# Kernel tuning notes

Measured on AMD Instinct MI355X. Metric: run time of the kernel, lower is better.

## Reference

```python
import jax, jax.numpy as jnp
import numpy as np

D_MODEL = 256
NUM_UNIVERSES = 8
D_UNIVERSE = D_MODEL // NUM_UNIVERSES
B, S = 1, 1024
TEMP = 5.0
NEG = -1e9


def setup_inputs() -> dict:
    key = jax.random.key(0)
    ks = jax.random.split(key, 5)
    scale = 1.0 / np.sqrt(D_MODEL)
    return {
        "x": jax.random.normal(ks[0], (B, S, D_MODEL), dtype=jnp.float32),
        "Wq": jax.random.normal(ks[1], (D_MODEL, D_MODEL), dtype=jnp.float32) * scale,
        "bq": jnp.zeros((D_MODEL,), dtype=jnp.float32),
        "Wk": jax.random.normal(ks[2], (D_MODEL, D_MODEL), dtype=jnp.float32) * scale,
        "bk": jnp.zeros((D_MODEL,), dtype=jnp.float32),
        "Wv": jax.random.normal(ks[3], (D_MODEL, D_MODEL), dtype=jnp.float32) * scale,
        "bv": jnp.zeros((D_MODEL,), dtype=jnp.float32),
        "Wo": jax.random.normal(ks[4], (D_MODEL, D_MODEL), dtype=jnp.float32) * scale,
        "bo": jnp.zeros((D_MODEL,), dtype=jnp.float32),
    }


def reference(x, Wq, bq, Wk, bk, Wv, bv, Wo, bo):
    b, s, d = x.shape
    h, du = NUM_UNIVERSES, D_UNIVERSE
    # Projections; Q,K squashed to [0,1] fuzzy truth values
    Q = jax.nn.sigmoid(x @ Wq + bq)
    K = jax.nn.sigmoid(x @ Wk + bk)
    V = x @ Wv + bv
    # [B,S,D] -> [B,H,S,du]
    Q = Q.reshape(b, s, h, du).transpose(0, 2, 1, 3)
    K = K.reshape(b, s, h, du).transpose(0, 2, 1, 3)
    V = V.reshape(b, s, h, du).transpose(0, 2, 1, 3)
    # Fuzzy implication: clamp(1 - Q_i + K_j, max=1), mean over d_universe
    # Broadcast to [B,H,S,S,du] (the memory-heavy intermediate)
    implication = jnp.minimum(1.0 - Q[:, :, :, None, :] + K[:, :, None, :, :], 1.0)
    truth = implication.mean(axis=-1)  # [B,H,S,S]
    # Causal mask
    causal = jnp.tril(jnp.ones((s, s), dtype=bool))
    truth = jnp.where(causal[None, None], truth, NEG)
    attn = jax.nn.softmax(truth * TEMP, axis=-1)
    out = jnp.einsum("bhij,bhjd->bhid", attn, V)
    out = out.transpose(0, 2, 1, 3).reshape(b, s, d)
    return out @ Wo + bo
```

## Files before the change

### kernel.cpp

```cpp
#include <hip/hip_runtime.h>
#include <hip/hip_bf16.h>
#include <math.h>

#define S_LEN 1024
#define DM    256
#define DU    32
#define TEMPF 5.0f
#define NS    4

typedef float f32x4  __attribute__((ext_vector_type(4)));
typedef short bf16x8 __attribute__((ext_vector_type(8)));

__device__ __forceinline__ unsigned short f32_to_bf16_rne(float x) {
    unsigned int b = __float_as_uint(x);
    b += 0x7FFFu + ((b >> 16) & 1u);
    return (unsigned short)(b >> 16);
}

__global__ __launch_bounds__(256) void qkv_proj_kernel(
    const float* __restrict__ x,
    const float* __restrict__ Wq, const float* __restrict__ bq,
    const float* __restrict__ Wk, const float* __restrict__ bk,
    const float* __restrict__ Wv, const float* __restrict__ bv,
    float* __restrict__ qo, float* __restrict__ ko, float* __restrict__ vo)
{
    const int mat = blockIdx.z;
    const float* __restrict__ W    = (mat == 0) ? Wq : ((mat == 1) ? Wk : Wv);
    const float* __restrict__ bias = (mat == 0) ? bq : ((mat == 1) ? bk : bv);
    float* __restrict__ dst        = (mat == 0) ? qo : ((mat == 1) ? ko : vo);

    const int n0 = blockIdx.x * 64;
    const int m0 = blockIdx.y * 32;
    const int t  = threadIdx.x;
    const int tx = t & 15;
    const int ty = t >> 4;

    __shared__ float xs[2][32][36];
    __shared__ float wsh[2][32][68];

    float acc[2][4] = {};

    const int xrow = t & 31;
    const int xkc  = (t >> 5) * 4;
    const int wrow = t >> 4;
    const int wcol = (t & 15) * 4;

    float4 xa = *(const float4*)&x[(m0 + xrow) * DM + xkc];
    float4 wa = *(const float4*)&W[wrow * DM + n0 + wcol];
    float4 wb = *(const float4*)&W[(wrow + 16) * DM + n0 + wcol];
    xs[0][xkc + 0][xrow] = xa.x; xs[0][xkc + 1][xrow] = xa.y;
    xs[0][xkc + 2][xrow] = xa.z; xs[0][xkc + 3][xrow] = xa.w;
    *(float4*)&wsh[0][wrow][wcol]      = wa;
    *(float4*)&wsh[0][wrow + 16][wcol] = wb;
    __syncthreads();

    int cur = 0;
    for (int k0 = 32; k0 < DM; k0 += 32) {
        xa = *(const float4*)&x[(m0 + xrow) * DM + k0 + xkc];
        wa = *(const float4*)&W[(k0 + wrow) * DM + n0 + wcol];
        wb = *(const float4*)&W[(k0 + wrow + 16) * DM + n0 + wcol];
        #pragma unroll
        for (int kk = 0; kk < 32; kk++) {
            float2 a2 = *(const float2*)&xs[cur][kk][ty * 2];
            float4 b4 = *(const float4*)&wsh[cur][kk][tx * 4];
            acc[0][0] += a2.x * b4.x; acc[0][1] += a2.x * b4.y;
            acc[0][2] += a2.x * b4.z; acc[0][3] += a2.x * b4.w;
            acc[1][0] += a2.y * b4.x; acc[1][1] += a2.y * b4.y;
            acc[1][2] += a2.y * b4.z; acc[1][3] += a2.y * b4.w;
        }
        const int nxt = cur ^ 1;
        xs[nxt][xkc + 0][xrow] = xa.x; xs[nxt][xkc + 1][xrow] = xa.y;
        xs[nxt][xkc + 2][xrow] = xa.z; xs[nxt][xkc + 3][xrow] = xa.w;
        *(float4*)&wsh[nxt][wrow][wcol]      = wa;
        *(float4*)&wsh[nxt][wrow + 16][wcol] = wb;
        __syncthreads();
        cur = nxt;
    }
    #pragma unroll
    for (int kk = 0; kk < 32; kk++) {
        float2 a2 = *(const float2*)&xs[cur][kk][ty * 2];
        float4 b4 = *(const float4*)&wsh[cur][kk][tx * 4];
        acc[0][0] += a2.x * b4.x; acc[0][1] += a2.x * b4.y;
        acc[0][2] += a2.x * b4.z; acc[0][3] += a2.x * b4.w;
        acc[1][0] += a2.y * b4.x; acc[1][1] += a2.y * b4.y;
        acc[1][2] += a2.y * b4.z; acc[1][3] += a2.y * b4.w;
    }

    #pragma unroll
    for (int j = 0; j < 4; j++) {
        const int cidx = n0 + tx * 4 + j;
        const float bb = bias[cidx];
        const int hh = cidx >> 5;
        const int dd = cidx & 31;
        #pragma unroll
        for (int i = 0; i < 2; i++) {
            const int row = m0 + ty * 2 + i;
            float val = acc[i][j] + bb;
            if (mat < 2) val = 1.0f / (1.0f + __expf(-val));
            dst[hh * (S_LEN * DU) + row * DU + dd] = val;
        }
    }
}

__global__ __launch_bounds__(256, 2) void attn_kernel(
    const float* __restrict__ q, const float* __restrict__ k,
    const float* __restrict__ v,
    float* __restrict__ part_o, float* __restrict__ part_l)
{
    const int bid = blockIdx.x;
    const int it4 = 15 - (bid >> 5);
    const int sub = bid & 31;
    const int h   = sub & 7;
    const int s   = sub >> 3;
    const int t   = threadIdx.x;
    const int r   = t >> 4;
    const int c   = t & 15;
    const int w   = t >> 6;
    const int i0  = it4 * 64;

    __shared__ __align__(16) float          Ks[64][36];
    __shared__ __align__(16) unsigned short Vt[32][88];
    __shared__ __align__(16) unsigned short Ps[64][88];

    float qreg[4][32];
    #pragma unroll
    for (int kq = 0; kq < 4; kq++) {
        const float* qrow = q + h * (S_LEN * DU) + (i0 + r + 16 * kq) * DU;
        #pragma unroll
        for (int d4 = 0; d4 < 8; d4++) {
            float4 qv = *(const float4*)&qrow[d4 * 4];
            qreg[kq][d4*4+0] = qv.x; qreg[kq][d4*4+1] = qv.y;
            qreg[kq][d4*4+2] = qv.z; qreg[kq][d4*4+3] = qv.w;
        }
    }

    float lpart[4] = {0.0f, 0.0f, 0.0f, 0.0f};
    f32x4 acc0 = {0.0f, 0.0f, 0.0f, 0.0f};
    f32x4 acc1 = {0.0f, 0.0f, 0.0f, 0.0f};

    const int jr = t >> 2;
    const int d0 = (t & 3) * 8;
    const float* kbase = k + h * (S_LEN * DU);
    const float* vbase = v + h * (S_LEN * DU);

    const int lane = t & 63;
    const int m    = lane & 15;
    const int quad = lane >> 4;

    const int njt = it4 + 1;
    float4 ka, kb, va, vb;
    if (s < njt) {
        const float* kp = kbase + (s * 64 + jr) * DU + d0;
        const float* vp = vbase + (s * 64 + jr) * DU + d0;
        ka = *(const float4*)kp; kb = *(const float4*)(kp + 4);
        va = *(const float4*)vp; vb = *(const float4*)(vp + 4);
    }

    for (int jt = s; jt < njt; jt += NS) {
        __syncthreads();
        *(float4*)&Ks[jr][d0]     = ka;
        *(float4*)&Ks[jr][d0 + 4] = kb;
        {
            float vv[8] = {va.x, va.y, va.z, va.w, vb.x, vb.y, vb.z, vb.w};
            #pragma unroll
            for (int i = 0; i < 8; i++)
                Vt[d0 + i][jr] = f32_to_bf16_rne(vv[i]);
        }
        __syncthreads();
        if (jt + NS < njt) {
            const float* kp = kbase + ((jt + NS) * 64 + jr) * DU + d0;
            const float* vp = vbase + ((jt + NS) * 64 + jr) * DU + d0;
            ka = *(const float4*)kp; kb = *(const float4*)(kp + 4);
            va = *(const float4*)vp; vb = *(const float4*)(vp + 4);
        }

        #pragma unroll
        for (int q4 = 0; q4 < 4; q4++) {
            const int jj  = c + q4 * 16;
            const int jgl = jt * 64 + jj;
            float sacc[4] = {0.0f, 0.0f, 0.0f, 0.0f};
            #pragma unroll
            for (int d = 0; d < 32; d += 4) {
                float4 k4 = *(const float4*)&Ks[jj][d];
                #pragma unroll
                for (int kq = 0; kq < 4; kq++) {
                    sacc[kq] += fmaxf(qreg[kq][d+0] - k4.x, 0.0f)
                              + fmaxf(qreg[kq][d+1] - k4.y, 0.0f)
                              + fmaxf(qreg[kq][d+2] - k4.z, 0.0f)
                              + fmaxf(qreg[kq][d+3] - k4.w, 0.0f);
                }
            }
            #pragma unroll
            for (int kq = 0; kq < 4; kq++) {
                const int ig = i0 + r + 16 * kq;
                const float p = (jgl <= ig)
                    ? __expf(TEMPF - (TEMPF / 32.0f) * sacc[kq]) : 0.0f;
                lpart[kq] += p;
                Ps[r + 16 * kq][jj] = f32_to_bf16_rne(p);
            }
        }
        __syncthreads();

        #pragma unroll
        for (int kc = 0; kc < 2; kc++) {
            bf16x8 a  = *(const bf16x8*)&Ps[16 * w + m][kc * 32 + quad * 8];
            bf16x8 b0 = *(const bf16x8*)&Vt[m]     [kc * 32 + quad * 8];
            bf16x8 b1 = *(const bf16x8*)&Vt[m + 16][kc * 32 + quad * 8];
            acc0 = __builtin_amdgcn_mfma_f32_16x16x32_bf16(a, b0, acc0, 0, 0, 0);
            acc1 = __builtin_amdgcn_mfma_f32_16x16x32_bf16(a, b1, acc1, 0, 0, 0);
        }
    }

    #pragma unroll
    for (int off = 8; off; off >>= 1)
        #pragma unroll
        for (int kq = 0; kq < 4; kq++)
            lpart[kq] += __shfl_xor(lpart[kq], off, 16);

    const int pbase = (h * 16 + it4) * NS + s;
    float* po = part_o + (size_t)pbase * 2048;
    #pragma unroll
    for (int reg = 0; reg < 4; reg++) {
        const int row = 16 * w + quad * 4 + reg;
        po[row * 32 + m]      = acc0[reg];
        po[row * 32 + m + 16] = acc1[reg];
    }
    if (c == 0) {
        #pragma unroll
        for (int kq = 0; kq < 4; kq++)
            part_l[pbase * 64 + r + 16 * kq] = lpart[kq];
    }
}

__global__ __launch_bounds__(256) void combine_kernel(
    const float* __restrict__ part_o, const float* __restrict__ part_l,
    float* __restrict__ attn)
{
    const int h    = blockIdx.x & 7;
    const int it4  = blockIdx.x >> 3;
    const int t    = threadIdx.x;
    const int r    = t >> 4;
    const int c    = t & 15;
    const int base = (h * 16 + it4) * NS;

    #pragma unroll
    for (int kq = 0; kq < 4; kq++) {
        const int row = r + 16 * kq;
        float os0 = 0.0f, os1 = 0.0f, ls = 0.0f;
        #pragma unroll
        for (int s2 = 0; s2 < NS; s2++) {
            const float* po = part_o + (size_t)(base + s2) * 2048;
            os0 += po[row * 32 + c];
            os1 += po[row * 32 + c + 16];
            ls  += part_l[(base + s2) * 64 + row];
        }
        const float inv = 1.0f / ls;
        attn[(it4 * 64 + row) * DM + h * DU + c]      = os0 * inv;
        attn[(it4 * 64 + row) * DM + h * DU + c + 16] = os1 * inv;
    }
}

__global__ __launch_bounds__(256) void out_proj_kernel(
    const float* __restrict__ a, const float* __restrict__ W,
    const float* __restrict__ bias, float* __restrict__ dst)
{
    const int n0 = blockIdx.x * 32;
    const int m0 = blockIdx.y * 32;
    const int t  = threadIdx.x;
    const int tx = t & 15;
    const int ty = t >> 4;

    __shared__ float xs[2][32][36];
    __shared__ float wsh[2][32][36];

    float acc[2][2] = {};

    const int arow = t & 31;
    const int akc  = (t >> 5) * 4;
    const int wr   = t >> 3;
    const int wc   = (t & 7) * 4;

    float4 xa = *(const float4*)&a[(m0 + arow) * DM + akc];
    float4 wa = *(const float4*)&W[wr * DM + n0 + wc];
    xs[0][akc + 0][arow] = xa.x; xs[0][akc + 1][arow] = xa.y;
    xs[0][akc + 2][arow] = xa.z; xs[0][akc + 3][arow] = xa.w;
    *(float4*)&wsh[0][wr][wc] = wa;
    __syncthreads();

    int cur = 0;
    for (int k0 = 32; k0 < DM; k0 += 32) {
        xa = *(const float4*)&a[(m0 + arow) * DM + k0 + akc];
        wa = *(const float4*)&W[(k0 + wr) * DM + n0 + wc];
        #pragma unroll
        for (int kk = 0; kk < 32; kk++) {
            float2 a2 = *(const float2*)&xs[cur][kk][ty * 2];
            float2 b2 = *(const float2*)&wsh[cur][kk][tx * 2];
            acc[0][0] += a2.x * b2.x; acc[0][1] += a2.x * b2.y;
            acc[1][0] += a2.y * b2.x; acc[1][1] += a2.y * b2.y;
        }
        const int nxt = cur ^ 1;
        xs[nxt][akc + 0][arow] = xa.x; xs[nxt][akc + 1][arow] = xa.y;
        xs[nxt][akc + 2][arow] = xa.z; xs[nxt][akc + 3][arow] = xa.w;
        *(float4*)&wsh[nxt][wr][wc] = wa;
        __syncthreads();
        cur = nxt;
    }
    #pragma unroll
    for (int kk = 0; kk < 32; kk++) {
        float2 a2 = *(const float2*)&xs[cur][kk][ty * 2];
        float2 b2 = *(const float2*)&wsh[cur][kk][tx * 2];
        acc[0][0] += a2.x * b2.x; acc[0][1] += a2.x * b2.y;
        acc[1][0] += a2.y * b2.x; acc[1][1] += a2.y * b2.y;
    }

    #pragma unroll
    for (int j = 0; j < 2; j++) {
        const int cidx = n0 + tx * 2 + j;
        const float bb = bias[cidx];
        #pragma unroll
        for (int i = 0; i < 2; i++) {
            const int row = m0 + ty * 2 + i;
            dst[row * DM + cidx] = acc[i][j] + bb;
        }
    }
}

extern "C" void kernel_launch(void* const* d_in, const int* in_sizes, int n_in,
                              void* d_out, int out_size, void* d_ws, size_t ws_size,
                              hipStream_t stream)
{
    const float* x  = (const float*)d_in[0];
    const float* Wq = (const float*)d_in[1];
    const float* bq = (const float*)d_in[2];
    const float* Wk = (const float*)d_in[3];
    const float* bk = (const float*)d_in[4];
    const float* Wv = (const float*)d_in[5];
    const float* bv = (const float*)d_in[6];
    const float* Wo = (const float*)d_in[7];
    const float* bo = (const float*)d_in[8];
    float* out = (float*)d_out;

    float* ws      = (float*)d_ws;
    float* q       = ws;
    float* k       = q + 262144;
    float* v       = k + 262144;
    float* attn    = v + 262144;
    float* part_o  = attn + 262144;
    float* part_l  = part_o + 1048576;

    qkv_proj_kernel<<<dim3(4, 32, 3), 256, 0, stream>>>(x, Wq, bq, Wk, bk, Wv, bv, q, k, v);
    attn_kernel<<<dim3(512), 256, 0, stream>>>(q, k, v, part_o, part_l);
    combine_kernel<<<dim3(128), 256, 0, stream>>>(part_o, part_l, attn);
    out_proj_kernel<<<dim3(8, 32), 256, 0, stream>>>(attn, Wo, bo, out);
}
```

Before: 111.8 us.

## Use split-bf16 MFMA for projections and fuse split-K combine into output projection

The QKV and output projections move from scalar FP32 FMA to MFMA 16x16x32 bf16 instructions. Each operand is split into high and low bf16 parts and three MFMAs are issued per tile, keeping close to FP32 accuracy. The separate combine kernel is removed: the output projection now sums the split-K partial outputs and normalizers directly while loading its A tiles, which saves one launch and a round trip through the attn buffer. Larger 64x64 tiles mean fewer blocks, and the combine work is repeated across the four column blocks.

```diff
diff --git a/kernel.cpp b/kernel.cpp
--- a/kernel.cpp
+++ b/kernel.cpp
@@ -15,6 +15,12 @@
     unsigned int b = __float_as_uint(x);
     b += 0x7FFFu + ((b >> 16) & 1u);
     return (unsigned short)(b >> 16);
+}
+
+__device__ __forceinline__ void split_bf16(float f, unsigned short& h, unsigned short& l) {
+    h = f32_to_bf16_rne(f);
+    float hf = __uint_as_float((unsigned int)h << 16);
+    l = f32_to_bf16_rne(f - hf);
 }
 
 __global__ __launch_bounds__(256) void qkv_proj_kernel(
@@ -24,80 +30,108 @@
     const float* __restrict__ Wv, const float* __restrict__ bv,
     float* __restrict__ qo, float* __restrict__ ko, float* __restrict__ vo)
 {
-    const int mat = blockIdx.z;
+    const int n0g = blockIdx.x * 64;
+    const int mat = n0g >> 8;
+    const int n0  = n0g & 255;
     const float* __restrict__ W    = (mat == 0) ? Wq : ((mat == 1) ? Wk : Wv);
     const float* __restrict__ bias = (mat == 0) ? bq : ((mat == 1) ? bk : bv);
     float* __restrict__ dst        = (mat == 0) ? qo : ((mat == 1) ? ko : vo);
 
-    const int n0 = blockIdx.x * 64;
-    const int m0 = blockIdx.y * 32;
-    const int t  = threadIdx.x;
-    const int tx = t & 15;
-    const int ty = t >> 4;
-
-    __shared__ float xs[2][32][36];
-    __shared__ float wsh[2][32][68];
-
-    float acc[2][4] = {};
-
-    const int xrow = t & 31;
-    const int xkc  = (t >> 5) * 4;
-    const int wrow = t >> 4;
-    const int wcol = (t & 15) * 4;
-
-    float4 xa = *(const float4*)&x[(m0 + xrow) * DM + xkc];
-    float4 wa = *(const float4*)&W[wrow * DM + n0 + wcol];
-    float4 wb = *(const float4*)&W[(wrow + 16) * DM + n0 + wcol];
-    xs[0][xkc + 0][xrow] = xa.x; xs[0][xkc + 1][xrow] = xa.y;
-    xs[0][xkc + 2][xrow] = xa.z; xs[0][xkc + 3][xrow] = xa.w;
-    *(float4*)&wsh[0][wrow][wcol]      = wa;
-    *(float4*)&wsh[0][wrow + 16][wcol] = wb;
+    const int m0   = blockIdx.y * 64;
+    const int t    = threadIdx.x;
+    const int w    = t >> 6;
+    const int lane = t & 63;
+    const int fm   = lane & 15;
+    const int quad = lane >> 4;
+    const int q8   = quad * 8;
+
+    __shared__ __align__(16) unsigned short Ah[2][64][40], Al[2][64][40];
+    __shared__ __align__(16) unsigned short Bh[2][64][40], Bl[2][64][40];
+
+    const int xr  = t >> 2;
+    const int xf  = (t & 3) * 8;
+    const int wn  = t & 63;
+    const int wkc = (t >> 6) * 8;
+
+    f32x4 acc[4];
+    #pragma unroll
+    for (int nt = 0; nt < 4; nt++)
+        #pragma unroll
+        for (int i = 0; i < 4; i++) acc[nt][i] = 0.0f;
+
+    const float* xbase = x + (m0 + xr) * DM + xf;
+    float xa[8], wv[8];
+
+    {
+        float4 a0 = *(const float4*)xbase;
+        float4 a1 = *(const float4*)(xbase + 4);
+        xa[0]=a0.x; xa[1]=a0.y; xa[2]=a0.z; xa[3]=a0.w;
+        xa[4]=a1.x; xa[5]=a1.y; xa[6]=a1.z; xa[7]=a1.w;
+        #pragma unroll
+        for (int i = 0; i < 8; i++) wv[i] = W[(wkc + i) * DM + n0 + wn];
+    }
+    {
+        bf16x8 vh, vl;
+        #pragma unroll
+        for (int i = 0; i < 8; i++) { unsigned short h,l; split_bf16(xa[i],h,l); vh[i]=(short)h; vl[i]=(short)l; }
+        *(bf16x8*)&Ah[0][xr][xf] = vh; *(bf16x8*)&Al[0][xr][xf] = vl;
+        #pragma unroll
+        for (int i = 0; i < 8; i++) { unsigned short h,l; split_bf16(wv[i],h,l); vh[i]=(short)h; vl[i]=(short)l; }
+        *(bf16x8*)&Bh[0][wn][wkc] = vh; *(bf16x8*)&Bl[0][wn][wkc] = vl;
+    }
     __syncthreads();
 
-    int cur = 0;
-    for (int k0 = 32; k0 < DM; k0 += 32) {
-        xa = *(const float4*)&x[(m0 + xrow) * DM + k0 + xkc];
-        wa = *(const float4*)&W[(k0 + wrow) * DM + n0 + wcol];
-        wb = *(const float4*)&W[(k0 + wrow + 16) * DM + n0 + wcol];
-        #pragma unroll
-        for (int kk = 0; kk < 32; kk++) {
-            float2 a2 = *(const float2*)&xs[cur][kk][ty * 2];
-            float4 b4 = *(const float4*)&wsh[cur][kk][tx * 4];
-            acc[0][0] += a2.x * b4.x; acc[0][1] += a2.x * b4.y;
-            acc[0][2] += a2.x * b4.z; acc[0][3] += a2.x * b4.w;
-            acc[1][0] += a2.y * b4.x; acc[1][1] += a2.y * b4.y;
-            acc[1][2] += a2.y * b4.z; acc[1][3] += a2.y * b4.w;
-        }
-        const int nxt = cur ^ 1;
-        xs[nxt][xkc + 0][xrow] = xa.x; xs[nxt][xkc + 1][xrow] = xa.y;
-        xs[nxt][xkc + 2][xrow] = xa.z; xs[nxt][xkc + 3][xrow] = xa.w;
-        *(float4*)&wsh[nxt][wrow][wcol]      = wa;
-        *(float4*)&wsh[nxt][wrow + 16][wcol] = wb;
-        __syncthreads();
-        cur = nxt;
-    }
-    #pragma unroll
-    for (int kk = 0; kk < 32; kk++) {
-        float2 a2 = *(const float2*)&xs[cur][kk][ty * 2];
-        float4 b4 = *(const float4*)&wsh[cur][kk][tx * 4];
-        acc[0][0] += a2.x * b4.x; acc[0][1] += a2.x * b4.y;
-        acc[0][2] += a2.x * b4.z; acc[0][3] += a2.x * b4.w;
-        acc[1][0] += a2.y * b4.x; acc[1][1] += a2.y * b4.y;
-        acc[1][2] += a2.y * b4.z; acc[1][3] += a2.y * b4.w;
-    }
-
-    #pragma unroll
-    for (int j = 0; j < 4; j++) {
-        const int cidx = n0 + tx * 4 + j;
-        const float bb = bias[cidx];
-        const int hh = cidx >> 5;
-        const int dd = cidx & 31;
-        #pragma unroll
-        for (int i = 0; i < 2; i++) {
-            const int row = m0 + ty * 2 + i;
-            float val = acc[i][j] + bb;
+    int buf = 0;
+    for (int step = 0; step < 8; step++) {
+        if (step < 7) {
+            const float* xp = xbase + (step + 1) * 32;
+            float4 a0 = *(const float4*)xp;
+            float4 a1 = *(const float4*)(xp + 4);
+            xa[0]=a0.x; xa[1]=a0.y; xa[2]=a0.z; xa[3]=a0.w;
+            xa[4]=a1.x; xa[5]=a1.y; xa[6]=a1.z; xa[7]=a1.w;
+            #pragma unroll
+            for (int i = 0; i < 8; i++)
+                wv[i] = W[((step + 1) * 32 + wkc + i) * DM + n0 + wn];
+        }
+        {
+            bf16x8 ah = *(const bf16x8*)&Ah[buf][16 * w + fm][q8];
+            bf16x8 al = *(const bf16x8*)&Al[buf][16 * w + fm][q8];
+            #pragma unroll
+            for (int nt = 0; nt < 4; nt++) {
+                bf16x8 bh = *(const bf16x8*)&Bh[buf][nt * 16 + fm][q8];
+                bf16x8 bl = *(const bf16x8*)&Bl[buf][nt * 16 + fm][q8];
+                acc[nt] = __builtin_amdgcn_mfma_f32_16x16x32_bf16(ah, bh, acc[nt], 0, 0, 0);
+                acc[nt] = __builtin_amdgcn_mfma_f32_16x16x32_bf16(al, bh, acc[nt], 0, 0, 0);
+                acc[nt] = __builtin_amdgcn_mfma_f32_16x16x32_bf16(ah, bl, acc[nt], 0, 0, 0);
+            }
+        }
+        if (step < 7) {
+            const int nb = buf ^ 1;
+            bf16x8 vh, vl;
+            #pragma unroll
+            for (int i = 0; i < 8; i++) { unsigned short h,l; split_bf16(xa[i],h,l); vh[i]=(short)h; vl[i]=(short)l; }
+            *(bf16x8*)&Ah[nb][xr][xf] = vh; *(bf16x8*)&Al[nb][xr][xf] = vl;
+            #pragma unroll
+            for (int i = 0; i < 8; i++) { unsigned short h,l; split_bf16(wv[i],h,l); vh[i]=(short)h; vl[i]=(short)l; }
+            *(bf16x8*)&Bh[nb][wn][wkc] = vh; *(bf16x8*)&Bl[nb][wn][wkc] = vl;
+            __syncthreads();
+            buf = nb;
+        }
+    }
+
+    #pragma unroll
+    for (int nt = 0; nt < 4; nt++) {
+        const int col = n0 + nt * 16 + fm;
+        const float bb = bias[col];
+        const int hh = col >> 5;
+        const int dd = col & 31;
+        float* dp = dst + hh * (S_LEN * DU) + dd;
+        #pragma unroll
+        for (int reg = 0; reg < 4; reg++) {
+            const int row = m0 + 16 * w + quad * 4 + reg;
+            float val = acc[nt][reg] + bb;
             if (mat < 2) val = 1.0f / (1.0f + __expf(-val));
-            dst[hh * (S_LEN * DU) + row * DU + dd] = val;
+            dp[row * DU] = val;
         }
     }
 }
@@ -232,95 +266,103 @@
     }
 }
 
-__global__ __launch_bounds__(256) void combine_kernel(
+__global__ __launch_bounds__(256) void out_proj_kernel(
     const float* __restrict__ part_o, const float* __restrict__ part_l,
-    float* __restrict__ attn)
+    const float* __restrict__ W, const float* __restrict__ bias,
+    float* __restrict__ dst)
 {
-    const int h    = blockIdx.x & 7;
-    const int it4  = blockIdx.x >> 3;
+    const int n0  = blockIdx.x * 64;
+    const int it4 = blockIdx.y;
+    const int m0  = it4 * 64;
     const int t    = threadIdx.x;
-    const int r    = t >> 4;
-    const int c    = t & 15;
-    const int base = (h * 16 + it4) * NS;
-
-    #pragma unroll
-    for (int kq = 0; kq < 4; kq++) {
-        const int row = r + 16 * kq;
-        float os0 = 0.0f, os1 = 0.0f, ls = 0.0f;
+    const int w    = t >> 6;
+    const int lane = t & 63;
+    const int fm   = lane & 15;
+    const int quad = lane >> 4;
+    const int q8   = quad * 8;
+
+    __shared__ __align__(16) unsigned short Ah[2][64][40], Al[2][64][40];
+    __shared__ __align__(16) unsigned short Bh[2][64][40], Bl[2][64][40];
+
+    const int xr  = t >> 2;
+    const int xf  = (t & 3) * 8;
+    const int wn  = t & 63;
+    const int wkc = (t >> 6) * 8;
+
+    f32x4 acc[4];
+    #pragma unroll
+    for (int nt = 0; nt < 4; nt++)
+        #pragma unroll
+        for (int i = 0; i < 4; i++) acc[nt][i] = 0.0f;
+
+    float xa[8], wv[8];
+
+    auto loadA = [&](int h) {
+        const int base = (h * 16 + it4) * NS;
+        float o[8] = {0,0,0,0,0,0,0,0};
+        float l = 0.0f;
         #pragma unroll
         for (int s2 = 0; s2 < NS; s2++) {
-            const float* po = part_o + (size_t)(base + s2) * 2048;
-            os0 += po[row * 32 + c];
-            os1 += po[row * 32 + c + 16];
-            ls  += part_l[(base + s2) * 64 + row];
-        }
-        const float inv = 1.0f / ls;
-        attn[(it4 * 64 + row) * DM + h * DU + c]      = os0 * inv;
-        attn[(it4 * 64 + row) * DM + h * DU + c + 16] = os1 * inv;
-    }
-}
-
-__global__ __launch_bounds__(256) void out_proj_kernel(
-    const float* __restrict__ a, const float* __restrict__ W,
-    const float* __restrict__ bias, float* __restrict__ dst)
-{
-    const int n0 = blockIdx.x * 32;
-    const int m0 = blockIdx.y * 32;
-    const int t  = threadIdx.x;
-    const int tx = t & 15;
-    const int ty = t >> 4;
-
-    __shared__ float xs[2][32][36];
-    __shared__ float wsh[2][32][36];
-
-    float acc[2][2] = {};
-
-    const int arow = t & 31;
-    const int akc  = (t >> 5) * 4;
-    const int wr   = t >> 3;
-    const int wc   = (t & 7) * 4;
-
-    float4 xa = *(const float4*)&a[(m0 + arow) * DM + akc];
-    float4 wa = *(const float4*)&W[wr * DM + n0 + wc];
-    xs[0][akc + 0][arow] = xa.x; xs[0][akc + 1][arow] = xa.y;
-    xs[0][akc + 2][arow] = xa.z; xs[0][akc + 3][arow] = xa.w;
-    *(float4*)&wsh[0][wr][wc] = wa;
+            const float* po = part_o + (size_t)(base + s2) * 2048 + xr * 32 + xf;
+            float4 p0 = *(const float4*)po;
+            float4 p1 = *(const float4*)(po + 4);
+            o[0]+=p0.x; o[1]+=p0.y; o[2]+=p0.z; o[3]+=p0.w;
+            o[4]+=p1.x; o[5]+=p1.y; o[6]+=p1.z; o[7]+=p1.w;
+            l += part_l[(base + s2) * 64 + xr];
+        }
+        const float inv = 1.0f / l;
+        #pragma unroll
+        for (int i = 0; i < 8; i++) xa[i] = o[i] * inv;
+    };
+    auto loadW = [&](int k0) {
+        #pragma unroll
+        for (int i = 0; i < 8; i++) wv[i] = W[(k0 + wkc + i) * DM + n0 + wn];
+    };
+    auto storeT = [&](int b) {
+        bf16x8 vh, vl;
+        #pragma unroll
+        for (int i = 0; i < 8; i++) { unsigned short h,l; split_bf16(xa[i],h,l); vh[i]=(short)h; vl[i]=(short)l; }
+        *(bf16x8*)&Ah[b][xr][xf] = vh; *(bf16x8*)&Al[b][xr][xf] = vl;
+        #pragma unroll
+        for (int i = 0; i < 8; i++) { unsigned short h,l; split_bf16(wv[i],h,l); vh[i]=(short)h; vl[i]=(short)l; }
+        *(bf16x8*)&Bh[b][wn][wkc] = vh; *(bf16x8*)&Bl[b][wn][wkc] = vl;
+    };
+
+    loadA(0); loadW(0);
+    storeT(0);
     __syncthreads();
 
-    int cur = 0;
-    for (int k0 = 32; k0 < DM; k0 += 32) {
-        xa = *(const float4*)&a[(m0 + arow) * DM + k0 + akc];
-        wa = *(const float4*)&W[(k0 + wr) * DM + n0 + wc];
-        #pragma unroll
-        for (int kk = 0; kk < 32; kk++) {
-            float2 a2 = *(const float2*)&xs[cur][kk][ty * 2];
-            float2 b2 = *(const float2*)&wsh[cur][kk][tx * 2];
-            acc[0][0] += a2.x * b2.x; acc[0][1] += a2.x * b2.y;
-            acc[1][0] += a2.y * b2.x; acc[1][1] += a2.y * b2.y;
-        }
-        const int nxt = cur ^ 1;
-        xs[nxt][akc + 0][arow] = xa.x; xs[nxt][akc + 1][arow] = xa.y;
-        xs[nxt][akc + 2][arow] = xa.z; xs[nxt][akc + 3][arow] = xa.w;
-        *(float4*)&wsh[nxt][wr][wc] = wa;
-        __syncthreads();
-        cur = nxt;
-    }
-    #pragma unroll
-    for (int kk = 0; kk < 32; kk++) {
-        float2 a2 = *(const float2*)&xs[cur][kk][ty * 2];
-        float2 b2 = *(const float2*)&wsh[cur][kk][tx * 2];
-        acc[0][0] += a2.x * b2.x; acc[0][1] += a2.x * b2.y;
-        acc[1][0] += a2.y * b2.x; acc[1][1] += a2.y * b2.y;
-    }
-
-    #pragma unroll
-    for (int j = 0; j < 2; j++) {
-        const int cidx = n0 + tx * 2 + j;
-        const float bb = bias[cidx];
-        #pragma unroll
-        for (int i = 0; i < 2; i++) {
-            const int row = m0 + ty * 2 + i;
-            dst[row * DM + cidx] = acc[i][j] + bb;
+    int buf = 0;
+    for (int step = 0; step < 8; step++) {
+        if (step < 7) { loadA(step + 1); loadW((step + 1) * 32); }
+        {
+            bf16x8 ah = *(const bf16x8*)&Ah[buf][16 * w + fm][q8];
+            bf16x8 al = *(const bf16x8*)&Al[buf][16 * w + fm][q8];
+            #pragma unroll
+            for (int nt = 0; nt < 4; nt++) {
+                bf16x8 bh = *(const bf16x8*)&Bh[buf][nt * 16 + fm][q8];
+                bf16x8 bl = *(const bf16x8*)&Bl[buf][nt * 16 + fm][q8];
+                acc[nt] = __builtin_amdgcn_mfma_f32_16x16x32_bf16(ah, bh, acc[nt], 0, 0, 0);
+                acc[nt] = __builtin_amdgcn_mfma_f32_16x16x32_bf16(al, bh, acc[nt], 0, 0, 0);
+                acc[nt] = __builtin_amdgcn_mfma_f32_16x16x32_bf16(ah, bl, acc[nt], 0, 0, 0);
+            }
+        }
+        if (step < 7) {
+            const int nb = buf ^ 1;
+            storeT(nb);
+            __syncthreads();
+            buf = nb;
+        }
+    }
+
+    #pragma unroll
+    for (int nt = 0; nt < 4; nt++) {
+        const int col = n0 + nt * 16 + fm;
+        const float bb = bias[col];
+        #pragma unroll
+        for (int reg = 0; reg < 4; reg++) {
+            const int row = m0 + 16 * w + quad * 4 + reg;
+            dst[row * DM + col] = acc[nt][reg] + bb;
         }
     }
 }
@@ -344,12 +386,10 @@
     float* q       = ws;
     float* k       = q + 262144;
     float* v       = k + 262144;
-    float* attn    = v + 262144;
-    float* part_o  = attn + 262144;
+    float* part_o  = v + 262144;
     float* part_l  = part_o + 1048576;
 
-    qkv_proj_kernel<<<dim3(4, 32, 3), 256, 0, stream>>>(x, Wq, bq, Wk, bk, Wv, bv, q, k, v);
+    qkv_proj_kernel<<<dim3(12, 16), 256, 0, stream>>>(x, Wq, bq, Wk, bk, Wv, bv, q, k, v);
     attn_kernel<<<dim3(512), 256, 0, stream>>>(q, k, v, part_o, part_l);
-    combine_kernel<<<dim3(128), 256, 0, stream>>>(part_o, part_l, attn);
-    out_proj_kernel<<<dim3(8, 32), 256, 0, stream>>>(attn, Wo, bo, out);
-}
+    out_proj_kernel<<<dim3(4, 16), 256, 0, stream>>>(part_o, part_l, Wo, bo, out);
+}
```

Result: faster. 109.2 us (-2.3%).
